# Kernel optimization log

Hardware: AMD Instinct MI355X
Metric: run time of the kernel (lower is better)

Reference implementation:

```python
import jax, jax.numpy as jnp
import numpy as np

VOLUME_SIZE = 48  # max_disp / down = 192 / 4


def setup_inputs() -> dict:
    key = jax.random.key(0)
    k1, k2 = jax.random.split(key)
    b, c, h, w = 8, 128, 128, 240
    left_feature = jax.random.normal(k1, (b, c, h, w), dtype=jnp.float32)
    right_feature = jax.random.normal(k2, (b, c, h, w), dtype=jnp.float32)
    return {"left_feature": left_feature, "right_feature": right_feature}


def reference(left_feature, right_feature):
    # cost_volume[:, i, :, x] = mean_c(L[:, :, :, x] * R[:, :, :, x-i]) for x >= i, else 0
    b, c, h, w = left_feature.shape
    col = jnp.arange(w)

    def per_disp(i):
        # shift right feature right by i; zero out wrapped-around columns (< i)
        r_shift = jnp.roll(right_feature, i, axis=-1)  # [b,c,h,w]
        prod_mean = jnp.mean(left_feature * r_shift, axis=1)  # [b,h,w]
        return jnp.where(col >= i, prod_mean, 0.0)

    cv = jax.vmap(per_disp)(jnp.arange(VOLUME_SIZE))  # [V,b,h,w]
    return jnp.transpose(cv, (1, 0, 2, 3))  # [b,V,h,w]
```

## Files before the change

### kernel.cpp

```cpp
#include <hip/hip_runtime.h>

#define CV_B 8
#define CV_C 128
#define CV_H 128
#define CV_W 240
#define CV_V 48
#define BSTRIDE 17

typedef __attribute__((ext_vector_type(8))) short bf16x8;
typedef __attribute__((ext_vector_type(4))) float f32x4;

__device__ __forceinline__ unsigned int pack2_bf16(float f0, float f1) {
    unsigned int u0 = __float_as_uint(f0);
    unsigned int u1 = __float_as_uint(f1);
    u0 += 0x7fffu + ((u0 >> 16) & 1u);
    u1 += 0x7fffu + ((u1 >> 16) & 1u);
    return (u0 >> 16) | (u1 & 0xffff0000u);
}

__device__ __forceinline__ bf16x8 pack8(const float v[8]) {
    union { unsigned int u[4]; bf16x8 h; } cv;
    cv.u[0] = pack2_bf16(v[0], v[1]);
    cv.u[1] = pack2_bf16(v[2], v[3]);
    cv.u[2] = pack2_bf16(v[4], v[5]);
    cv.u[3] = pack2_bf16(v[6], v[7]);
    return cv.h;
}

__global__ __launch_bounds__(256, 4) void cost_volume_kernel(
        const float* __restrict__ Lf, const float* __restrict__ Rf,
        float* __restrict__ out)
{
    __shared__ float band[4][2][CV_V * BSTRIDE];

    const int t    = threadIdx.x;
    const int wv   = t >> 6;
    const int lane = t & 63;
    const int n    = lane & 15;
    const int quad = lane >> 4;

    const int half = blockIdx.x;
    const int y    = blockIdx.y;
    const int b    = blockIdx.z;

    const int T0 = half * 8 + wv * 2;
    const int nt = (T0 + 1 < 15) ? 2 : 1;
    const int x0 = T0 * 16;

    const int plane = CV_H * CV_W;
    const float* Lrow = Lf + (b * CV_C) * plane + y * CV_W;
    const float* Rrow = Rf + (b * CV_C) * plane + y * CV_W;

    const int kbase = quad * 8;

    bf16x8 aF[2][4];
#pragma unroll
    for (int e = 0; e < 2; ++e) {
        if (e < nt) {
            const float* p = Lrow + x0 + 16 * e + n;
#pragma unroll
            for (int ks = 0; ks < 4; ++ks) {
                float v[8];
#pragma unroll
                for (int jj = 0; jj < 8; ++jj)
                    v[jj] = p[(ks * 32 + kbase + jj) * plane];
                aF[e][ks] = pack8(v);
            }
        }
    }

    float* band0 = &band[wv][0][0];
    float* band1 = &band[wv][1][0];

    for (int w = T0 - 3; w <= T0 + nt - 1; ++w) {
        const int j0 = 16 * w;
        const int jg = j0 + n;
        const bool ok = (jg >= 0);
        const float* p = Rrow + jg;

        bf16x8 bF[4];
#pragma unroll
        for (int ks = 0; ks < 4; ++ks) {
            float v[8];
#pragma unroll
            for (int jj = 0; jj < 8; ++jj)
                v[jj] = ok ? p[(ks * 32 + kbase + jj) * plane] : 0.0f;
            bF[ks] = pack8(v);
        }

#pragma unroll
        for (int e = 0; e < 2; ++e) {
            if (e < nt && w >= T0 + e - 3 && w <= T0 + e) {
                f32x4 acc = {0.f, 0.f, 0.f, 0.f};
#pragma unroll
                for (int ks = 0; ks < 4; ++ks)
                    acc = __builtin_amdgcn_mfma_f32_16x16x32_bf16(aF[e][ks], bF[ks], acc, 0, 0, 0);
                float* bd = e ? band1 : band0;
                const int ibase = 16 * (T0 + e - w);
#pragma unroll
                for (int r = 0; r < 4; ++r) {
                    const int xloc = quad * 4 + r;
                    const int i    = ibase + xloc - n;
                    if (i >= 0 && i < CV_V)
                        bd[i * BSTRIDE + xloc] = acc[r] * (1.0f / 128.0f);
                }
            }
        }
    }

#pragma unroll
    for (int e = 0; e < 2; ++e) {
        if (e < nt) {
            const float* bd = e ? band1 : band0;
            const int xb = x0 + 16 * e;
#pragma unroll
            for (int uu = 0; uu < 12; ++uu) {
                const int idx = lane + uu * 64;
                const int i   = idx >> 4;
                const int xx  = idx & 15;
                out[((b * CV_V + i) * CV_H + y) * CV_W + xb + xx] = bd[i * BSTRIDE + xx];
            }
        }
    }
}

extern "C" void kernel_launch(void* const* d_in, const int* in_sizes, int n_in,
                              void* d_out, int out_size, void* d_ws, size_t ws_size,
                              hipStream_t stream)
{
    const float* Lf = (const float*)d_in[0];
    const float* Rf = (const float*)d_in[1];
    float* o = (float*)d_out;
    dim3 grid(2, CV_H, CV_B);
    dim3 block(256);
    hipLaunchKernelGGL(cost_volume_kernel, grid, block, 0, stream, Lf, Rf, o);
}
```

Baseline: 305.4 us.

## Replace MFMA banded cost volume with shared-memory fp16 packed FMA kernel

Replaces the bf16 MFMA tile approach with a per-row block that stages L and R channel pairs as half2 in shared memory, with double-buffered register prefetch across four channel chunks. Each thread computes 4 columns by 12 disparities using packed half2 FMAs and writes float4 outputs directly, dropping the band transpose buffer. The intent is to remove the redundant strided global loads and wasted MFMA work on out-of-band tiles. The cost is fp16 accumulation over 64 channel pairs per lane, which risks precision loss, and the block tile and grid shape also change.

```diff
diff --git a/kernel.cpp b/kernel.cpp
--- a/kernel.cpp
+++ b/kernel.cpp
@@ -1,125 +1,127 @@
 #include <hip/hip_runtime.h>
+#include <hip/hip_fp16.h>
 
 #define CV_B 8
 #define CV_C 128
 #define CV_H 128
 #define CV_W 240
 #define CV_V 48
-#define BSTRIDE 17
+#define PLANE (CV_H * CV_W)
+#define GUARD 48
+#define ROWW (GUARD + CV_W)
+#define NCP 16
+#define NCHUNK 4
 
-typedef __attribute__((ext_vector_type(8))) short bf16x8;
-typedef __attribute__((ext_vector_type(4))) float f32x4;
-
-__device__ __forceinline__ unsigned int pack2_bf16(float f0, float f1) {
-    unsigned int u0 = __float_as_uint(f0);
-    unsigned int u1 = __float_as_uint(f1);
-    u0 += 0x7fffu + ((u0 >> 16) & 1u);
-    u1 += 0x7fffu + ((u1 >> 16) & 1u);
-    return (u0 >> 16) | (u1 & 0xffff0000u);
-}
-
-__device__ __forceinline__ bf16x8 pack8(const float v[8]) {
-    union { unsigned int u[4]; bf16x8 h; } cv;
-    cv.u[0] = pack2_bf16(v[0], v[1]);
-    cv.u[1] = pack2_bf16(v[2], v[3]);
-    cv.u[2] = pack2_bf16(v[4], v[5]);
-    cv.u[3] = pack2_bf16(v[6], v[7]);
-    return cv.h;
-}
-
-__global__ __launch_bounds__(256, 4) void cost_volume_kernel(
+__global__ __launch_bounds__(256, 3) void cost_volume_kernel(
         const float* __restrict__ Lf, const float* __restrict__ Rf,
         float* __restrict__ out)
 {
-    __shared__ float band[4][2][CV_V * BSTRIDE];
+    __shared__ __align__(16) __half2 sBuf[2][NCP][ROWW];
 
-    const int t    = threadIdx.x;
-    const int wv   = t >> 6;
-    const int lane = t & 63;
-    const int n    = lane & 15;
-    const int quad = lane >> 4;
+    const int t  = threadIdx.x;
+    const int y  = blockIdx.x;
+    const int b  = blockIdx.y;
+    const int wv = t >> 6;
+    const int u  = t & 63;
+    const bool act = (u < 60);
 
-    const int half = blockIdx.x;
-    const int y    = blockIdx.y;
-    const int b    = blockIdx.z;
+    const float* Lrow = Lf + (size_t)(b * CV_C) * PLANE + y * CV_W;
+    const float* Rrow = Rf + (size_t)(b * CV_C) * PLANE + y * CV_W;
 
-    const int T0 = half * 8 + wv * 2;
-    const int nt = (T0 + 1 < 15) ? 2 : 1;
-    const int x0 = T0 * 16;
+    const int side = wv >> 1;
+    const int a0   = (wv & 1) * 8;
+    const float* Srow = side ? Rrow : Lrow;
 
-    const int plane = CV_H * CV_W;
-    const float* Lrow = Lf + (b * CV_C) * plane + y * CV_W;
-    const float* Rrow = Rf + (b * CV_C) * plane + y * CV_W;
+    for (int idx = t; idx < 2 * NCP * GUARD; idx += 256) {
+        const int s  = idx / (NCP * GUARD);
+        const int rm = idx % (NCP * GUARD);
+        sBuf[s][rm / GUARD][rm % GUARD] = __floats2half2_rn(0.f, 0.f);
+    }
 
-    const int kbase = quad * 8;
+    float4 f0[8], f1[8];
+    if (act) {
+#pragma unroll
+        for (int q = 0; q < 8; ++q) {
+            const float* p = Srow + (size_t)(2 * (a0 + q)) * PLANE + 4 * u;
+            f0[q] = *(const float4*)p;
+            f1[q] = *(const float4*)(p + PLANE);
+        }
+#pragma unroll
+        for (int q = 0; q < 8; ++q) {
+            union { float4 v; __half2 h[4]; } wbuf;
+            wbuf.h[0] = __floats2half2_rn(f0[q].x, f1[q].x);
+            wbuf.h[1] = __floats2half2_rn(f0[q].y, f1[q].y);
+            wbuf.h[2] = __floats2half2_rn(f0[q].z, f1[q].z);
+            wbuf.h[3] = __floats2half2_rn(f0[q].w, f1[q].w);
+            *(float4*)&sBuf[side][a0 + q][GUARD + 4 * u] = wbuf.v;
+        }
+    }
+    __syncthreads();
 
-    bf16x8 aF[2][4];
+    __half2 acc[4][12];
 #pragma unroll
-    for (int e = 0; e < 2; ++e) {
-        if (e < nt) {
-            const float* p = Lrow + x0 + 16 * e + n;
+    for (int xx = 0; xx < 4; ++xx)
 #pragma unroll
-            for (int ks = 0; ks < 4; ++ks) {
-                float v[8];
+        for (int r = 0; r < 12; ++r) acc[xx][r] = __floats2half2_rn(0.f, 0.f);
+
+    const int baseL = GUARD + 4 * u;
+    const int baseR = GUARD - 12 - 12 * wv + 4 * u;
+
+    for (int k = 0; k < NCHUNK; ++k) {
+        const bool pf = (k + 1 < NCHUNK);
+        if (pf && act) {
 #pragma unroll
-                for (int jj = 0; jj < 8; ++jj)
-                    v[jj] = p[(ks * 32 + kbase + jj) * plane];
-                aF[e][ks] = pack8(v);
+            for (int q = 0; q < 8; ++q) {
+                const float* p = Srow + (size_t)((k + 1) * 32 + 2 * (a0 + q)) * PLANE + 4 * u;
+                f0[q] = *(const float4*)p;
+                f1[q] = *(const float4*)(p + PLANE);
             }
         }
-    }
 
-    float* band0 = &band[wv][0][0];
-    float* band1 = &band[wv][1][0];
-
-    for (int w = T0 - 3; w <= T0 + nt - 1; ++w) {
-        const int j0 = 16 * w;
-        const int jg = j0 + n;
-        const bool ok = (jg >= 0);
-        const float* p = Rrow + jg;
-
-        bf16x8 bF[4];
+        if (act) {
 #pragma unroll
-        for (int ks = 0; ks < 4; ++ks) {
-            float v[8];
+            for (int cp = 0; cp < NCP; ++cp) {
+                union { float4 v; __half2 h[4]; } lv, rw[4];
+                lv.v = *(const float4*)&sBuf[0][cp][baseL];
 #pragma unroll
-            for (int jj = 0; jj < 8; ++jj)
-                v[jj] = ok ? p[(ks * 32 + kbase + jj) * plane] : 0.0f;
-            bF[ks] = pack8(v);
-        }
-
+                for (int kk = 0; kk < 4; ++kk)
+                    rw[kk].v = *(const float4*)&sBuf[1][cp][baseR + 4 * kk];
 #pragma unroll
-        for (int e = 0; e < 2; ++e) {
-            if (e < nt && w >= T0 + e - 3 && w <= T0 + e) {
-                f32x4 acc = {0.f, 0.f, 0.f, 0.f};
+                for (int r = 0; r < 12; ++r) {
 #pragma unroll
-                for (int ks = 0; ks < 4; ++ks)
-                    acc = __builtin_amdgcn_mfma_f32_16x16x32_bf16(aF[e][ks], bF[ks], acc, 0, 0, 0);
-                float* bd = e ? band1 : band0;
-                const int ibase = 16 * (T0 + e - w);
-#pragma unroll
-                for (int r = 0; r < 4; ++r) {
-                    const int xloc = quad * 4 + r;
-                    const int i    = ibase + xloc - n;
-                    if (i >= 0 && i < CV_V)
-                        bd[i * BSTRIDE + xloc] = acc[r] * (1.0f / 128.0f);
+                    for (int xx = 0; xx < 4; ++xx) {
+                        const int m = xx + 12 - r;
+                        acc[xx][r] = __hfma2(lv.h[xx], rw[m >> 2].h[m & 3], acc[xx][r]);
+                    }
                 }
             }
         }
+        __syncthreads();
+
+        if (pf && act) {
+#pragma unroll
+            for (int q = 0; q < 8; ++q) {
+                union { float4 v; __half2 h[4]; } wbuf;
+                wbuf.h[0] = __floats2half2_rn(f0[q].x, f1[q].x);
+                wbuf.h[1] = __floats2half2_rn(f0[q].y, f1[q].y);
+                wbuf.h[2] = __floats2half2_rn(f0[q].z, f1[q].z);
+                wbuf.h[3] = __floats2half2_rn(f0[q].w, f1[q].w);
+                *(float4*)&sBuf[side][a0 + q][GUARD + 4 * u] = wbuf.v;
+            }
+        }
+        __syncthreads();
     }
 
+    if (act) {
 #pragma unroll
-    for (int e = 0; e < 2; ++e) {
-        if (e < nt) {
-            const float* bd = e ? band1 : band0;
-            const int xb = x0 + 16 * e;
-#pragma unroll
-            for (int uu = 0; uu < 12; ++uu) {
-                const int idx = lane + uu * 64;
-                const int i   = idx >> 4;
-                const int xx  = idx & 15;
-                out[((b * CV_V + i) * CV_H + y) * CV_W + xb + xx] = bd[i * BSTRIDE + xx];
-            }
+        for (int r = 0; r < 12; ++r) {
+            const int i = 12 * wv + r;
+            float4 o;
+            o.x = (__low2float(acc[0][r]) + __high2float(acc[0][r])) * (1.f / 128.f);
+            o.y = (__low2float(acc[1][r]) + __high2float(acc[1][r])) * (1.f / 128.f);
+            o.z = (__low2float(acc[2][r]) + __high2float(acc[2][r])) * (1.f / 128.f);
+            o.w = (__low2float(acc[3][r]) + __high2float(acc[3][r])) * (1.f / 128.f);
+            *(float4*)&out[(((size_t)b * CV_V + i) * CV_H + y) * CV_W + 4 * u] = o;
         }
     }
 }
@@ -131,7 +133,7 @@
     const float* Lf = (const float*)d_in[0];
     const float* Rf = (const float*)d_in[1];
     float* o = (float*)d_out;
-    dim3 grid(2, CV_H, CV_B);
+    dim3 grid(CV_H, CV_B);
     dim3 block(256);
     hipLaunchKernelGGL(cost_volume_kernel, grid, block, 0, stream, Lf, Rf, o);
 }
```

New measurement: 287.5 us. 5.9% less time.
